# Performance work log

Hardware: AMD Instinct MI355X
Metric: run time of the kernel (lower is better)

The kernel has to match this reference:

```python
import jax, jax.numpy as jnp
import numpy as np

NEG = -1e30  # log-space 'zero'; avoids -inf - -inf NaNs in grads


def _skew(x, D, fill):
    """x: (B, T, U) -> (B, D, U) with skew[b, d, u] = x[b, d-u, u] (anti-diagonal layout)."""
    B, T, U = x.shape
    d = jnp.arange(D)[:, None]
    u = jnp.arange(U)[None, :]
    t = d - u
    valid = (t >= 0) & (t < T)
    g = x[:, jnp.clip(t, 0, T - 1), u]  # (B, D, U)
    return jnp.where(valid[None], g, fill)


def rnnt_loss(logits, targets, fbank_len, text_len, blank=0):
    """Per-sequence RNN-T negative log-likelihood via an anti-diagonal alpha DP.

    logits: (B, T, U+1, V); targets: (B, U+1) incl. SOS; lengths per sequence.
    """
    B, T, U1, V = logits.shape
    U = U1 - 1
    labels = targets[:, 1:]              # (B, U) -- drop SOS, matches targets[:, 1:]
    lab_len = text_len - 1               # (B,)   -- matches text_len - 1

    lp = jax.nn.log_softmax(logits, axis=-1)          # (B, T, U1, V)
    blank_lp = lp[..., blank]                          # (B, T, U1)
    emit_lp = jnp.take_along_axis(
        lp[:, :, :U, :], labels[:, None, :, None], axis=3
    )[..., 0]                                          # (B, T, U)

    D = T + U1 - 1                       # number of anti-diagonals d = t + u
    bsk = _skew(blank_lp, D, NEG)        # (B, D, U1): blank at (t, u) -> (t+u, u)
    esk = _skew(emit_lp, D, NEG)         # (B, D, U)

    # alpha[t, u] = logaddexp(alpha[t-1, u] + blank[t-1, u], alpha[t, u-1] + emit[t, u-1])
    # In skewed coords, diagonal d depends only on diagonal d-1.
    P0 = jnp.full((B, U1), NEG, dtype=logits.dtype).at[:, 0].set(0.0)

    def step(P, xs):
        bl, em = xs                      # (B, U1), (B, U) from diagonal d-1
        stay = P + bl                    # alpha[t-1, u] + blank[t-1, u]
        move = jnp.pad(P[:, :-1] + em, ((0, 0), (1, 0)), constant_values=NEG)
        new = jnp.logaddexp(stay, move)
        return new, new

    xs = (jnp.swapaxes(bsk, 0, 1)[:-1], jnp.swapaxes(esk, 0, 1)[:-1])  # (D-1, B, .)
    _, rest = jax.lax.scan(step, P0, xs)
    alphas = jnp.concatenate([P0[None], rest], axis=0)   # (D, B, U1)

    b = jnp.arange(B)
    d_fin = fbank_len - 1 + lab_len                      # final diagonal per seq
    a_fin = alphas[d_fin, b, lab_len]                    # alpha[T_b-1, U_b]
    bl_fin = blank_lp[b, fbank_len - 1, lab_len]         # final blank emission
    return -(a_fin + bl_fin)                             # (B,)


def setup_inputs() -> dict:
    key = jax.random.key(0)
    k1, k2, k3, k4 = jax.random.split(key, 4)
    B, T, U1, V = 8, 200, 101, 512
    logits = jax.random.normal(k1, (B, T, U1, V), dtype=jnp.float32)
    targets = jax.random.randint(k2, (B, U1), 1, V).astype(jnp.int32)  # non-blank labels
    fbank_len = jax.random.randint(k3, (B,), 150, T + 1).astype(jnp.int32)
    text_len = jax.random.randint(k4, (B,), 60, U1 + 1).astype(jnp.int32)
    return {"logits": logits, "targets": targets, "fbank_len": fbank_len, "text_len": text_len}


def reference(logits, targets, fbank_len, text_len):
    loss = rnnt_loss(logits, targets, fbank_len, text_len, blank=0)
    return loss.mean()  # reduction='mean'
```

## Files before the change

### kernel.cpp

```cpp
#include <hip/hip_runtime.h>

#define NEG (-1e30f)

constexpr int B  = 8;
constexpr int T  = 200;
constexpr int U1 = 101;
constexpr int U  = U1 - 1;
constexpr int V  = 512;

__device__ __forceinline__ float lae(float a, float b) {
    float m = fmaxf(a, b);
    float d = fabsf(a - b);
    return m + log1pf(__expf(-d));
}

__global__ __launch_bounds__(256) void lse_kernel(const float* __restrict__ logits,
                                                  const int*   __restrict__ targets,
                                                  float* __restrict__ blankT,
                                                  float* __restrict__ emitT) {
    const int wave = (blockIdx.x * 256 + threadIdx.x) >> 6;
    const int lane = threadIdx.x & 63;
    const int nrows = B * T * U1;
    if (wave >= nrows) return;

    const int b   = wave / (T * U1);
    const int rem = wave % (T * U1);
    const int t   = rem / U1;
    const int u   = rem % U1;

    const float* base = logits + (size_t)wave * V;

    const float4 x0 = *(const float4*)(base + lane * 4);
    const float4 x1 = *(const float4*)(base + 256 + lane * 4);

    float m = fmaxf(fmaxf(fmaxf(x0.x, x0.y), fmaxf(x0.z, x0.w)),
                    fmaxf(fmaxf(x1.x, x1.y), fmaxf(x1.z, x1.w)));
    #pragma unroll
    for (int off = 32; off; off >>= 1) m = fmaxf(m, __shfl_xor(m, off));

    float s = __expf(x0.x - m) + __expf(x0.y - m) + __expf(x0.z - m) + __expf(x0.w - m)
            + __expf(x1.x - m) + __expf(x1.y - m) + __expf(x1.z - m) + __expf(x1.w - m);
    #pragma unroll
    for (int off = 32; off; off >>= 1) s += __shfl_xor(s, off);

    const float lse = m + __logf(s);

    if (lane == 0) {
        blankT[((size_t)b * U1 + u) * T + t] = x0.x - lse;
        if (u < U) {
            const int lab = targets[b * U1 + u + 1];
            emitT[((size_t)b * U1 + u) * T + t] = base[lab] - lse;
        }
    }
}

__global__ __launch_bounds__(128) void dp_kernel(const float* __restrict__ blankT,
                                                 const float* __restrict__ emitT,
                                                 const int*   __restrict__ fbank_len,
                                                 const int*   __restrict__ text_len,
                                                 float* __restrict__ loss) {
    const int b = blockIdx.x;
    const int u = threadIdx.x;
    __shared__ float M[2][128];

    const int Tb   = fbank_len[b];
    const int L    = text_len[b] - 1;
    const int dfin = Tb - 1 + L;

    const bool has_b = (u < U1);
    const bool has_e = (u < U);
    const float* blc = blankT + ((size_t)b * U1 + (has_b ? u : 0)) * T;
    const float* emc = emitT  + ((size_t)b * U1 + (has_e ? u : 0)) * T;

    float p = (u == 0) ? 0.0f : NEG;

    int t0 = -u;
    float bl_n = (has_b && t0 >= 0 && t0 < T) ? blc[t0] : NEG;
    float em_n = (has_e && t0 >= 0 && t0 < T) ? emc[t0] : NEG;

    for (int d = 1; d <= dfin; ++d) {
        const float bl = bl_n;
        const float em = em_n;
        const int tn = d - u;
        bl_n = (has_b && tn >= 0 && tn < T) ? blc[tn] : NEG;
        em_n = (has_e && tn >= 0 && tn < T) ? emc[tn] : NEG;

        const int par = d & 1;
        M[par][u] = p + em;
        __syncthreads();
        const float mv = (u >= 1) ? M[par][u - 1] : NEG;
        p = lae(p + bl, mv);
    }

    if (u == L) {
        const float bl_fin = blc[Tb - 1];
        loss[b] = -(p + bl_fin);
    }
}

__global__ void mean_kernel(const float* __restrict__ loss, float* __restrict__ out) {
    if (threadIdx.x == 0) {
        float s = 0.0f;
        #pragma unroll
        for (int i = 0; i < B; ++i) s += loss[i];
        out[0] = s * (1.0f / B);
    }
}

extern "C" void kernel_launch(void* const* d_in, const int* in_sizes, int n_in,
                              void* d_out, int out_size, void* d_ws, size_t ws_size,
                              hipStream_t stream) {
    const float* logits  = (const float*)d_in[0];
    const int*   targets = (const int*)  d_in[1];
    const int*   fbank   = (const int*)  d_in[2];
    const int*   text    = (const int*)  d_in[3];

    float* ws     = (float*)d_ws;
    float* blankT = ws;
    float* emitT  = ws + (size_t)B * U1 * T;
    float* loss   = emitT + (size_t)B * U1 * T;

    const int nrows  = B * T * U1;
    const int nblk   = (nrows + 3) / 4;

    lse_kernel<<<nblk, 256, 0, stream>>>(logits, targets, blankT, emitT);
    dp_kernel<<<B, 128, 0, stream>>>(blankT, emitT, fbank, text, loss);
    mean_kernel<<<1, 64, 0, stream>>>(loss, (float*)d_out);
}
```

Measured before the change: 616.8 us.

## Skip out-of-length rows in softmax and run DP in one wave from LDS

The log-softmax kernel now returns early for rows with t beyond the sequence length or u beyond the label length, so it reads less of the logits tensor. The DP kernel stages each sequence's blank and emit tables in dynamic LDS (about 160 KB, which needs the max-dynamic-shared-memory attribute) and uses a single 64-lane wave with two u positions per lane. Neighbour values move through a wave shuffle, which removes the per-diagonal block barrier. log1pf is replaced by a fast log, which trades some accuracy for speed.

New measurement: 521.2 us. -15.5%, faster.

```diff
diff --git a/kernel.cpp b/kernel.cpp
--- a/kernel.cpp
+++ b/kernel.cpp
@@ -11,11 +11,13 @@
 __device__ __forceinline__ float lae(float a, float b) {
     float m = fmaxf(a, b);
     float d = fabsf(a - b);
-    return m + log1pf(__expf(-d));
+    return m + __logf(1.0f + __expf(-d));
 }
 
 __global__ __launch_bounds__(256) void lse_kernel(const float* __restrict__ logits,
                                                   const int*   __restrict__ targets,
+                                                  const int*   __restrict__ fbank_len,
+                                                  const int*   __restrict__ text_len,
                                                   float* __restrict__ blankT,
                                                   float* __restrict__ emitT) {
     const int wave = (blockIdx.x * 256 + threadIdx.x) >> 6;
@@ -27,6 +29,10 @@
     const int rem = wave % (T * U1);
     const int t   = rem / U1;
     const int u   = rem % U1;
+
+    const int Tb = fbank_len[b];
+    const int L  = text_len[b] - 1;
+    if (t >= Tb || u > L) return;
 
     const float* base = logits + (size_t)wave * V;
 
@@ -47,55 +53,77 @@
 
     if (lane == 0) {
         blankT[((size_t)b * U1 + u) * T + t] = x0.x - lse;
-        if (u < U) {
+        if (u < L) {
             const int lab = targets[b * U1 + u + 1];
             emitT[((size_t)b * U1 + u) * T + t] = base[lab] - lse;
         }
     }
 }
 
-__global__ __launch_bounds__(128) void dp_kernel(const float* __restrict__ blankT,
-                                                 const float* __restrict__ emitT,
-                                                 const int*   __restrict__ fbank_len,
-                                                 const int*   __restrict__ text_len,
-                                                 float* __restrict__ loss) {
+extern __shared__ float smem[];
+
+__global__ __launch_bounds__(64) void dp_kernel(const float* __restrict__ blankT,
+                                                const float* __restrict__ emitT,
+                                                const int*   __restrict__ fbank_len,
+                                                const int*   __restrict__ text_len,
+                                                float* __restrict__ loss) {
     const int b = blockIdx.x;
-    const int u = threadIdx.x;
-    __shared__ float M[2][128];
+    const int l = threadIdx.x;
+    const int u0 = 2 * l, u1 = 2 * l + 1;
 
     const int Tb   = fbank_len[b];
     const int L    = text_len[b] - 1;
     const int dfin = Tb - 1 + L;
 
-    const bool has_b = (u < U1);
-    const bool has_e = (u < U);
-    const float* blc = blankT + ((size_t)b * U1 + (has_b ? u : 0)) * T;
-    const float* emc = emitT  + ((size_t)b * U1 + (has_e ? u : 0)) * T;
+    float* sb = smem;
+    float* se = smem + U1 * T;
 
-    float p = (u == 0) ? 0.0f : NEG;
+    {
+        const float4* srcB = (const float4*)(blankT + (size_t)b * U1 * T);
+        const float4* srcE = (const float4*)(emitT  + (size_t)b * U1 * T);
+        float4* dstB = (float4*)sb;
+        float4* dstE = (float4*)se;
+        const int n4b = (L + 1) * (T / 4);
+        const int n4e = L * (T / 4);
+        for (int i = l; i < n4b; i += 64) dstB[i] = srcB[i];
+        for (int i = l; i < n4e; i += 64) dstE[i] = srcE[i];
+    }
+    __syncthreads();
 
-    int t0 = -u;
-    float bl_n = (has_b && t0 >= 0 && t0 < T) ? blc[t0] : NEG;
-    float em_n = (has_e && t0 >= 0 && t0 < T) ? emc[t0] : NEG;
+    const bool a0 = (u0 <= L), a1 = (u1 <= L);
+    const bool e0 = (u0 <  L), e1 = (u1 <  L);
+    const float* sb0 = sb + u0 * T; const float* sb1 = sb + u1 * T;
+    const float* se0 = se + u0 * T; const float* se1 = se + u1 * T;
+
+    float p0 = (u0 == 0) ? 0.0f : NEG;
+    float p1 = NEG;
+
+    int t0 = -u0;
+    float bl0 = (a0 && t0 >= 0 && t0 < Tb) ? sb0[t0] : NEG;
+    float em0 = (e0 && t0 >= 0 && t0 < Tb) ? se0[t0] : NEG;
+    float bl1 = NEG, em1 = NEG;
 
     for (int d = 1; d <= dfin; ++d) {
-        const float bl = bl_n;
-        const float em = em_n;
-        const int tn = d - u;
-        bl_n = (has_b && tn >= 0 && tn < T) ? blc[tn] : NEG;
-        em_n = (has_e && tn >= 0 && tn < T) ? emc[tn] : NEG;
+        const int ta = d - u0, tb2 = ta - 1;
+        const float nbl0 = (a0 && ta  >= 0 && ta  < Tb) ? sb0[ta]  : NEG;
+        const float nem0 = (e0 && ta  >= 0 && ta  < Tb) ? se0[ta]  : NEG;
+        const float nbl1 = (a1 && tb2 >= 0 && tb2 < Tb) ? sb1[tb2] : NEG;
+        const float nem1 = (e1 && tb2 >= 0 && tb2 < Tb) ? se1[tb2] : NEG;
 
-        const int par = d & 1;
-        M[par][u] = p + em;
-        __syncthreads();
-        const float mv = (u >= 1) ? M[par][u - 1] : NEG;
-        p = lae(p + bl, mv);
+        const float M1  = p1 + em1;
+        float mv0 = __shfl_up(M1, 1);
+        if (l == 0) mv0 = NEG;
+        const float mv1 = p0 + em0;
+
+        p0 = lae(p0 + bl0, mv0);
+        p1 = lae(p1 + bl1, mv1);
+
+        bl0 = nbl0; em0 = nem0; bl1 = nbl1; em1 = nem1;
     }
 
-    if (u == L) {
-        const float bl_fin = blc[Tb - 1];
-        loss[b] = -(p + bl_fin);
-    }
+    const float bl_fin = sb[L * T + (Tb - 1)];
+    if (u0 == L) loss[b] = -(p0 + bl_fin);
+    if (u1 == L) loss[b] = -(p1 + bl_fin);
 }
 
 __global__ void mean_kernel(const float* __restrict__ loss, float* __restrict__ out) {
@@ -120,10 +148,15 @@
     float* emitT  = ws + (size_t)B * U1 * T;
     float* loss   = emitT + (size_t)B * U1 * T;
 
-    const int nrows  = B * T * U1;
-    const int nblk   = (nrows + 3) / 4;
+    const int nrows = B * T * U1;
+    const int nblk  = (nrows + 3) / 4;
 
-    lse_kernel<<<nblk, 256, 0, stream>>>(logits, targets, blankT, emitT);
-    dp_kernel<<<B, 128, 0, stream>>>(blankT, emitT, fbank, text, loss);
+    const size_t dp_lds = (size_t)(U1 + U) * T * sizeof(float);
+    (void)hipFuncSetAttribute((const void*)dp_kernel,
+                              hipFuncAttributeMaxDynamicSharedMemorySize,
+                              (int)dp_lds);
+
+    lse_kernel<<<nblk, 256, 0, stream>>>(logits, targets, fbank, text, blankT, emitT);
+    dp_kernel<<<B, 64, dp_lds, stream>>>(blankT, emitT, fbank, text, loss);
     mean_kernel<<<1, 64, 0, stream>>>(loss, (float*)d_out);
 }
```
